# Performance work log

Measured on AMD Instinct MI355X. Metric: run time of the kernel, lower is better.

Reference implementation:

```python
import jax, jax.numpy as jnp
import numpy as np

NUM_EMBEDDINGS = 1024
EMBEDDING_DIM = 16
COMMITMENT_COST = 0.25
B, H, W = 16, 64, 64


def setup_inputs() -> dict:
    key = jax.random.key(0)
    k1, k2 = jax.random.split(key)
    z = jax.random.normal(k1, (B, H, W, EMBEDDING_DIM), dtype=jnp.float32)
    # nn.Embedding init: uniform(-1/num_embeddings, 1/num_embeddings)
    lim = 1.0 / NUM_EMBEDDINGS
    embedding_weight = jax.random.uniform(
        k2, (NUM_EMBEDDINGS, EMBEDDING_DIM), dtype=jnp.float32,
        minval=-lim, maxval=lim)
    return {"z": z, "embedding_weight": embedding_weight}


def reference(z, embedding_weight):
    b, h, w, c = z.shape
    flat_z = z.reshape(-1, c)  # [N, D]
    # squared L2 distances: ||z||^2 + ||e||^2 - 2 z.e
    distances = (
        jnp.sum(flat_z ** 2, axis=1, keepdims=True)
        + jnp.sum(embedding_weight ** 2, axis=1)
        - 2.0 * flat_z @ embedding_weight.T
    )  # [N, K]
    encoding_indices = jnp.argmin(distances, axis=1)  # [N]
    z_q = embedding_weight[encoding_indices].reshape(z.shape)
    loss = (
        jnp.mean((jax.lax.stop_gradient(z_q) - z) ** 2)
        + COMMITMENT_COST * jnp.mean((z_q - jax.lax.stop_gradient(z)) ** 2)
    )
    z_q_st = z + jax.lax.stop_gradient(z_q - z)  # straight-through
    return z_q_st, loss, encoding_indices.reshape(b, h, w)
```

## Files before the change

### kernel.cpp

```cpp
#include <hip/hip_runtime.h>
#include <string.h>


typedef __bf16 bf16x8 __attribute__((ext_vector_type(8)));
typedef float  f32x16 __attribute__((ext_vector_type(16)));

constexpr int BLOCK = 256;
constexpr int NROWS = 65536;
constexpr int K = 1024;
constexpr int RPB = 64;
constexpr int NBLK = NROWS / RPB;
constexpr int TPW = 16;
constexpr int CAP = 192;
constexpr float BAND = 1.5e-3f;
constexpr int OFF_LOSS = 1048576;
constexpr int OFF_IDX  = 1048577;

__device__ __forceinline__ float np_sumsq16(const float* a) {
  float s[16];
#pragma unroll
  for (int j = 0; j < 16; ++j) s[j] = __fmul_rn(a[j], a[j]);
  float r[8];
#pragma unroll
  for (int j = 0; j < 8; ++j) r[j] = __fadd_rn(s[j], s[j + 8]);
  const float t0 = __fadd_rn(r[0], r[1]);
  const float t1 = __fadd_rn(r[2], r[3]);
  const float t2 = __fadd_rn(r[4], r[5]);
  const float t3 = __fadd_rn(r[6], r[7]);
  return __fadd_rn(__fadd_rn(t0, t1), __fadd_rn(t2, t3));
}

__device__ __forceinline__ float np_dist(const float* zz, const float* ee,
                                         float z2, float e2k) {
  float c0 = zz[0]*ee[0];   c0 = fmaf(zz[1],ee[1],c0);   c0 = fmaf(zz[2],ee[2],c0);   c0 = fmaf(zz[3],ee[3],c0);
  float c1 = zz[4]*ee[4];   c1 = fmaf(zz[5],ee[5],c1);   c1 = fmaf(zz[6],ee[6],c1);   c1 = fmaf(zz[7],ee[7],c1);
  float c2 = zz[8]*ee[8];   c2 = fmaf(zz[9],ee[9],c2);   c2 = fmaf(zz[10],ee[10],c2); c2 = fmaf(zz[11],ee[11],c2);
  float c3 = zz[12]*ee[12]; c3 = fmaf(zz[13],ee[13],c3); c3 = fmaf(zz[14],ee[14],c3); c3 = fmaf(zz[15],ee[15],c3);
  const float dot = __fadd_rn(__fadd_rn(c0, c1), __fadd_rn(c2, c3));
  return __fmaf_rn(-2.0f, dot, __fadd_rn(z2, e2k));
}

__global__ __launch_bounds__(256)
void vq_pre(const float* __restrict__ emb, float* __restrict__ e2g,
            char* __restrict__ Bpack) {
  const int r = blockIdx.x * 256 + threadIdx.x;
  const float4* g4 = reinterpret_cast<const float4*>(emb);
  float ee[16];
  float4* ev = reinterpret_cast<float4*>(ee);
#pragma unroll
  for (int j = 0; j < 4; ++j) ev[j] = g4[r * 4 + j];
  e2g[r] = np_sumsq16(ee);
  unsigned int wd[8];
#pragma unroll
  for (int j = 0; j < 8; ++j) {
    __bf16 lo = (__bf16)ee[2*j], hi = (__bf16)ee[2*j+1];
    unsigned short ulo, uhi;
    memcpy(&ulo, &lo, 2); memcpy(&uhi, &hi, 2);
    wd[j] = (unsigned int)ulo | ((unsigned int)uhi << 16);
  }
  const int tt = r >> 5, c = r & 31;
  *reinterpret_cast<uint4*>(Bpack + tt*1024 + c*16)       = make_uint4(wd[0], wd[1], wd[2], wd[3]);
  *reinterpret_cast<uint4*>(Bpack + tt*1024 + 512 + c*16) = make_uint4(wd[4], wd[5], wd[6], wd[7]);
}

__global__ __launch_bounds__(BLOCK, 4)
void vq_main(const float* __restrict__ z, const float* __restrict__ emb,
             const float* __restrict__ e2g, const char* __restrict__ Bpack,
             float* __restrict__ out, float* __restrict__ partials) {
  __shared__ unsigned int sclist[4][CAP];
  __shared__ unsigned long long smin64[2][32];
  __shared__ float smin[4][32];
  __shared__ int   scnt[4];
  __shared__ float sred[4];

  const int t = threadIdx.x;
  const int lane = t & 63;
  const int w = t >> 6;
  const int pair = w >> 1;
  const int h = lane >> 5;
  const int rr = lane & 31;

  const float4* g4 = reinterpret_cast<const float4*>(emb);
  const float4* z4 = reinterpret_cast<const float4*>(z);

  if (lane == 0) scnt[w] = 0;
  if (t < 64) smin64[t >> 5][t & 31] = ~0ull;

  const int wrow0 = blockIdx.x * RPB + (w >> 1) * 32;
  const float* zrow = z + (size_t)(wrow0 + rr) * 16 + h * 8;
  const float4 a0 = *reinterpret_cast<const float4*>(zrow);
  const float4 a1 = *reinterpret_cast<const float4*>(zrow + 4);
  bf16x8 af;
  af[0]=(__bf16)a0.x; af[1]=(__bf16)a0.y; af[2]=(__bf16)a0.z; af[3]=(__bf16)a0.w;
  af[4]=(__bf16)a1.x; af[5]=(__bf16)a1.y; af[6]=(__bf16)a1.z; af[7]=(__bf16)a1.w;

  const int kt0 = (w & 1) * TPW;
  const bf16x8* bfp = reinterpret_cast<const bf16x8*>(Bpack + (size_t)lane * 16);

  float runm[16];
#pragma unroll
  for (int i = 0; i < 16; ++i) runm[i] = __builtin_inff();

#pragma unroll 4
  for (int tt = kt0; tt < kt0 + TPW; ++tt) {
    f32x16 zc = {};
    f32x16 acc = __builtin_amdgcn_mfma_f32_32x32x16_bf16(af, bfp[tt * 64], zc, 0, 0, 0);
    const float pre = e2g[tt * 32 + rr] + 0.5f;
#pragma unroll
    for (int i = 0; i < 16; ++i)
      runm[i] = fminf(runm[i], __fmaf_rn(-2.0f, acc[i], pre));
  }

#pragma unroll
  for (int i = 0; i < 16; ++i)
#pragma unroll
    for (int m = 1; m < 32; m <<= 1)
      runm[i] = fminf(runm[i], __shfl_xor(runm[i], m));

  if (rr == 0) {
#pragma unroll
    for (int i = 0; i < 16; ++i)
      smin[w][(i & 3) + 8 * (i >> 2) + 4 * h] = runm[i];
  }
  __syncthreads();
#pragma unroll
  for (int i = 0; i < 16; ++i)
    runm[i] = fminf(runm[i], smin[w ^ 1][(i & 3) + 8 * (i >> 2) + 4 * h]) + BAND;

#pragma unroll 4
  for (int tt = kt0; tt < kt0 + TPW; ++tt) {
    f32x16 zc = {};
    f32x16 acc = __builtin_amdgcn_mfma_f32_32x32x16_bf16(af, bfp[tt * 64], zc, 0, 0, 0);
    const float pre = e2g[tt * 32 + rr] + 0.5f;
    const int kcol = tt * 32 + rr;
#pragma unroll
    for (int i = 0; i < 16; ++i) {
      const float m = __fmaf_rn(-2.0f, acc[i], pre);
      if (m <= runm[i]) {
        const int rowloc = (i & 3) + 8 * (i >> 2) + 4 * h;
        const int slot = atomicAdd(&scnt[w], 1);
        if (slot < CAP) sclist[w][slot] = ((unsigned)rowloc << 16) | (unsigned)kcol;
      }
    }
  }
  int cnt = scnt[w]; if (cnt > CAP) cnt = CAP;

  for (int j0 = 0; j0 < cnt; j0 += 64) {
    const int j = j0 + lane;
    if (j < cnt) {
      const unsigned ent = sclist[w][j];
      const int rowj = (int)(ent >> 16), kj = (int)(ent & 1023);
      float zz[16]; float4* zv = reinterpret_cast<float4*>(zz);
#pragma unroll
      for (int q = 0; q < 4; ++q) zv[q] = z4[(size_t)(wrow0 + rowj) * 4 + q];
      float ee[16]; float4* ev = reinterpret_cast<float4*>(ee);
#pragma unroll
      for (int q = 0; q < 4; ++q) ev[q] = g4[(size_t)kj * 4 + q];
      const float d = np_dist(zz, ee, np_sumsq16(zz), e2g[kj]);
      const unsigned long long key =
          ((unsigned long long)__float_as_uint(d) << 32) | (unsigned long long)kj;
      atomicMin(&smin64[pair][rowj], key);
    }
  }
  __syncthreads();

  float lsum = 0.0f;
  if (!(w & 1) && lane < 32) {
    const int bk = (int)(smin64[pair][lane] & 1023ull);
    const int r = wrow0 + lane;
    float zz[16]; float4* zv = reinterpret_cast<float4*>(zz);
#pragma unroll
    for (int q = 0; q < 4; ++q) zv[q] = z4[(size_t)r * 4 + q];
    float ee[16]; float4* ev = reinterpret_cast<float4*>(ee);
#pragma unroll
    for (int q = 0; q < 4; ++q) ev[q] = g4[(size_t)bk * 4 + q];
    float ov[16];
#pragma unroll
    for (int j2 = 0; j2 < 16; ++j2) {
      const float d = __fsub_rn(ee[j2], zz[j2]);
      lsum = fmaf(d, d, lsum);
      ov[j2] = __fadd_rn(zz[j2], d);
    }
    float4* o4 = reinterpret_cast<float4*>(out) + (size_t)r * 4;
    const float4* ovv = reinterpret_cast<const float4*>(ov);
#pragma unroll
    for (int q = 0; q < 4; ++q) o4[q] = ovv[q];
    out[OFF_IDX + r] = (float)bk;
  }

#pragma unroll
  for (int off = 32; off > 0; off >>= 1) lsum += __shfl_down(lsum, off);
  if (lane == 0) sred[w] = lsum;
  __syncthreads();
  if (t == 0) partials[blockIdx.x] = (sred[0] + sred[1]) + (sred[2] + sred[3]);
}

__global__ __launch_bounds__(256)
void vq_fin(const float* __restrict__ partials, float* __restrict__ out) {
  const int t = threadIdx.x;
  float v = (partials[t] + partials[t + 256]) + (partials[t + 512] + partials[t + 768]);
#pragma unroll
  for (int off = 32; off > 0; off >>= 1) v += __shfl_down(v, off);
  __shared__ float s[4];
  if ((t & 63) == 0) s[t >> 6] = v;
  __syncthreads();
  if (t == 0) {
    const float S = (s[0] + s[1]) + (s[2] + s[3]);
    const float m = S / 1048576.0f;
    out[OFF_LOSS] = 1.25f * m;
  }
}

extern "C" void kernel_launch(void* const* d_in, const int* in_sizes, int n_in,
                              void* d_out, int out_size, void* d_ws, size_t ws_size,
                              hipStream_t stream) {
  const float* z   = reinterpret_cast<const float*>(d_in[0]);
  const float* emb = reinterpret_cast<const float*>(d_in[1]);
  float* out       = reinterpret_cast<float*>(d_out);
  float* e2g       = reinterpret_cast<float*>(d_ws);
  float* partials  = e2g + K;
  char*  Bpack     = reinterpret_cast<char*>(e2g + 2048);
  vq_pre <<<K / 256, 256, 0, stream>>>(emb, e2g, Bpack);
  vq_main<<<NBLK, BLOCK, 0, stream>>>(z, emb, e2g, Bpack, out, partials);
  vq_fin <<<1, 256, 0, stream>>>(partials, out);
}
```

Baseline: 37.01 us.

## Split codebook across four waves per 32-row block and double grid size

Each block now handles 32 rows instead of 64, and all four waves share the same rows, each scanning a quarter of the codebook tiles. The cross-wave minimum becomes a four-way reduction, and per-tile e2 norms are preloaded into registers. Only one wave does the epilogue and writes the partial loss directly, which removes a barrier. The grid doubles to 2048 blocks with a higher occupancy target, trading more blocks and duplicated z loads for shorter per-wave MFMA chains and more parallelism.

```diff
diff --git a/kernel.cpp b/kernel.cpp
--- a/kernel.cpp
+++ b/kernel.cpp
@@ -8,10 +8,10 @@
 constexpr int BLOCK = 256;
 constexpr int NROWS = 65536;
 constexpr int K = 1024;
-constexpr int RPB = 64;
+constexpr int RPB = 32;
 constexpr int NBLK = NROWS / RPB;
-constexpr int TPW = 16;
-constexpr int CAP = 192;
+constexpr int TPW = 8;
+constexpr int CAP = 96;
 constexpr float BAND = 1.5e-3f;
 constexpr int OFF_LOSS = 1048576;
 constexpr int OFF_IDX  = 1048577;
@@ -63,20 +63,18 @@
   *reinterpret_cast<uint4*>(Bpack + tt*1024 + 512 + c*16) = make_uint4(wd[4], wd[5], wd[6], wd[7]);
 }
 
-__global__ __launch_bounds__(BLOCK, 4)
+__global__ __launch_bounds__(BLOCK, 8)
 void vq_main(const float* __restrict__ z, const float* __restrict__ emb,
              const float* __restrict__ e2g, const char* __restrict__ Bpack,
              float* __restrict__ out, float* __restrict__ partials) {
   __shared__ unsigned int sclist[4][CAP];
-  __shared__ unsigned long long smin64[2][32];
-  __shared__ float smin[4][32];
+  __shared__ unsigned long long smin64[RPB];
+  __shared__ float smin[4][RPB];
   __shared__ int   scnt[4];
-  __shared__ float sred[4];
 
   const int t = threadIdx.x;
   const int lane = t & 63;
   const int w = t >> 6;
-  const int pair = w >> 1;
   const int h = lane >> 5;
   const int rr = lane & 31;
 
@@ -84,9 +82,9 @@
   const float4* z4 = reinterpret_cast<const float4*>(z);
 
   if (lane == 0) scnt[w] = 0;
-  if (t < 64) smin64[t >> 5][t & 31] = ~0ull;
-
-  const int wrow0 = blockIdx.x * RPB + (w >> 1) * 32;
+  if (t < RPB) smin64[t] = ~0ull;
+
+  const int wrow0 = blockIdx.x * RPB;
   const float* zrow = z + (size_t)(wrow0 + rr) * 16 + h * 8;
   const float4 a0 = *reinterpret_cast<const float4*>(zrow);
   const float4 a1 = *reinterpret_cast<const float4*>(zrow + 4);
@@ -94,8 +92,12 @@
   af[0]=(__bf16)a0.x; af[1]=(__bf16)a0.y; af[2]=(__bf16)a0.z; af[3]=(__bf16)a0.w;
   af[4]=(__bf16)a1.x; af[5]=(__bf16)a1.y; af[6]=(__bf16)a1.z; af[7]=(__bf16)a1.w;
 
-  const int kt0 = (w & 1) * TPW;
+  const int kt0 = w * TPW;
   const bf16x8* bfp = reinterpret_cast<const bf16x8*>(Bpack + (size_t)lane * 16);
+
+  float e2r[TPW];
+#pragma unroll
+  for (int j = 0; j < TPW; ++j) e2r[j] = e2g[(kt0 + j) * 32 + rr] + 0.5f;
 
   float runm[16];
 #pragma unroll
@@ -105,7 +107,7 @@
   for (int tt = kt0; tt < kt0 + TPW; ++tt) {
     f32x16 zc = {};
     f32x16 acc = __builtin_amdgcn_mfma_f32_32x32x16_bf16(af, bfp[tt * 64], zc, 0, 0, 0);
-    const float pre = e2g[tt * 32 + rr] + 0.5f;
+    const float pre = e2r[tt - kt0];
 #pragma unroll
     for (int i = 0; i < 16; ++i)
       runm[i] = fminf(runm[i], __fmaf_rn(-2.0f, acc[i], pre));
@@ -124,14 +126,17 @@
   }
   __syncthreads();
 #pragma unroll
-  for (int i = 0; i < 16; ++i)
-    runm[i] = fminf(runm[i], smin[w ^ 1][(i & 3) + 8 * (i >> 2) + 4 * h]) + BAND;
+  for (int i = 0; i < 16; ++i) {
+    const int pr = (i & 3) + 8 * (i >> 2) + 4 * h;
+    runm[i] = fminf(fminf(smin[0][pr], smin[1][pr]),
+                    fminf(smin[2][pr], smin[3][pr])) + BAND;
+  }
 
 #pragma unroll 4
   for (int tt = kt0; tt < kt0 + TPW; ++tt) {
     f32x16 zc = {};
     f32x16 acc = __builtin_amdgcn_mfma_f32_32x32x16_bf16(af, bfp[tt * 64], zc, 0, 0, 0);
-    const float pre = e2g[tt * 32 + rr] + 0.5f;
+    const float pre = e2r[tt - kt0];
     const int kcol = tt * 32 + rr;
 #pragma unroll
     for (int i = 0; i < 16; ++i) {
@@ -159,46 +164,48 @@
       const float d = np_dist(zz, ee, np_sumsq16(zz), e2g[kj]);
       const unsigned long long key =
           ((unsigned long long)__float_as_uint(d) << 32) | (unsigned long long)kj;
-      atomicMin(&smin64[pair][rowj], key);
+      atomicMin(&smin64[rowj], key);
     }
   }
   __syncthreads();
 
-  float lsum = 0.0f;
-  if (!(w & 1) && lane < 32) {
-    const int bk = (int)(smin64[pair][lane] & 1023ull);
-    const int r = wrow0 + lane;
-    float zz[16]; float4* zv = reinterpret_cast<float4*>(zz);
-#pragma unroll
-    for (int q = 0; q < 4; ++q) zv[q] = z4[(size_t)r * 4 + q];
-    float ee[16]; float4* ev = reinterpret_cast<float4*>(ee);
-#pragma unroll
-    for (int q = 0; q < 4; ++q) ev[q] = g4[(size_t)bk * 4 + q];
-    float ov[16];
-#pragma unroll
-    for (int j2 = 0; j2 < 16; ++j2) {
-      const float d = __fsub_rn(ee[j2], zz[j2]);
-      lsum = fmaf(d, d, lsum);
-      ov[j2] = __fadd_rn(zz[j2], d);
+  if (t < 64) {
+    float lsum = 0.0f;
+    if (lane < 32) {
+      const int bk = (int)(smin64[lane] & 1023ull);
+      const int r = wrow0 + lane;
+      float zz[16]; float4* zv = reinterpret_cast<float4*>(zz);
+#pragma unroll
+      for (int q = 0; q < 4; ++q) zv[q] = z4[(size_t)r * 4 + q];
+      float ee[16]; float4* ev = reinterpret_cast<float4*>(ee);
+#pragma unroll
+      for (int q = 0; q < 4; ++q) ev[q] = g4[(size_t)bk * 4 + q];
+      float ov[16];
+#pragma unroll
+      for (int j2 = 0; j2 < 16; ++j2) {
+        const float d = __fsub_rn(ee[j2], zz[j2]);
+        lsum = fmaf(d, d, lsum);
+        ov[j2] = __fadd_rn(zz[j2], d);
+      }
+      float4* o4 = reinterpret_cast<float4*>(out) + (size_t)r * 4;
+      const float4* ovv = reinterpret_cast<const float4*>(ov);
+#pragma unroll
+      for (int q = 0; q < 4; ++q) o4[q] = ovv[q];
+      out[OFF_IDX + r] = (float)bk;
     }
-    float4* o4 = reinterpret_cast<float4*>(out) + (size_t)r * 4;
-    const float4* ovv = reinterpret_cast<const float4*>(ov);
-#pragma unroll
-    for (int q = 0; q < 4; ++q) o4[q] = ovv[q];
-    out[OFF_IDX + r] = (float)bk;
-  }
-
-#pragma unroll
-  for (int off = 32; off > 0; off >>= 1) lsum += __shfl_down(lsum, off);
-  if (lane == 0) sred[w] = lsum;
-  __syncthreads();
-  if (t == 0) partials[blockIdx.x] = (sred[0] + sred[1]) + (sred[2] + sred[3]);
+#pragma unroll
+    for (int off = 32; off > 0; off >>= 1) lsum += __shfl_down(lsum, off);
+    if (lane == 0) partials[blockIdx.x] = lsum;
+  }
 }
 
 __global__ __launch_bounds__(256)
 void vq_fin(const float* __restrict__ partials, float* __restrict__ out) {
   const int t = threadIdx.x;
-  float v = (partials[t] + partials[t + 256]) + (partials[t + 512] + partials[t + 768]);
+  float v = 0.0f;
+#pragma unroll
+  for (int j = 0; j < NBLK / 256; ++j)
+    v += partials[t + 256 * j];
 #pragma unroll
   for (int off = 32; off > 0; off >>= 1) v += __shfl_down(v, off);
   __shared__ float s[4];
@@ -219,7 +226,7 @@
   float* out       = reinterpret_cast<float*>(d_out);
   float* e2g       = reinterpret_cast<float*>(d_ws);
   float* partials  = e2g + K;
-  char*  Bpack     = reinterpret_cast<char*>(e2g + 2048);
+  char*  Bpack     = reinterpret_cast<char*>(e2g + 3072);
   vq_pre <<<K / 256, 256, 0, stream>>>(emb, e2g, Bpack);
   vq_main<<<NBLK, BLOCK, 0, stream>>>(z, emb, e2g, Bpack, out, partials);
   vq_fin <<<1, 256, 0, stream>>>(partials, out);
```

New measurement: 43.32 us. 1.17x slower.
